# Kernel tuning notes

Hardware: AMD Instinct MI355X
Metric: run time of the kernel (lower is better)

## Reference

```python
import jax, jax.numpy as jnp
import numpy as np

B, N, D, H = 32, 64, 64, 4
E = 4 * D
HD = E // H
EPS = 1e-10
TAU = 1.0


def _ln(x, g, b, eps=1e-5):
    m = x.mean(-1, keepdims=True)
    v = ((x - m) ** 2).mean(-1, keepdims=True)
    return (x - m) * jax.lax.rsqrt(v + eps) * g + b


def setup_inputs() -> dict:
    key = jax.random.key(0)
    ks = jax.random.split(key, 8)
    x = jax.random.normal(ks[0], (B, N, D), jnp.float32)
    A = jax.random.normal(ks[1], (B, N, N, 2 * D), jnp.float32)
    attn_mask = jax.random.randint(ks[2], (B, N, N), 0, 2).astype(jnp.int32)
    gumbel_u = jax.random.uniform(ks[3], (B, N, H, N), jnp.float32, minval=1e-6, maxval=1.0)
    in_proj_w = (jax.random.normal(ks[4], (3 * E, E), jnp.float32) * (E ** -0.5))
    in_proj_b = jnp.zeros((3 * E,), jnp.float32)
    w1 = jax.random.normal(ks[5], (HD, HD), jnp.float32) * (HD ** -0.5)
    b1 = jnp.zeros((HD,), jnp.float32)
    w2 = jax.random.normal(ks[6], (1, HD), jnp.float32) * (HD ** -0.5)
    b2 = jnp.zeros((1,), jnp.float32)
    return dict(x=x, A=A, attn_mask=attn_mask, gumbel_u=gumbel_u,
                ln_node_g=jnp.ones((D,), jnp.float32), ln_node_b=jnp.zeros((D,), jnp.float32),
                ln_edge_g=jnp.ones((2 * D,), jnp.float32), ln_edge_b=jnp.zeros((2 * D,), jnp.float32),
                in_proj_w=in_proj_w, in_proj_b=in_proj_b, w1=w1, b1=b1, w2=w2, b2=b2)


def reference(x, A, attn_mask, gumbel_u, ln_node_g, ln_node_b, ln_edge_g, ln_edge_b,
              in_proj_w, in_proj_b, w1, b1, w2, b2):
    b, n, d = x.shape
    e = 4 * d
    hd = e // H
    mask = attn_mask.astype(x.dtype)                      # (b, target, neighbor), 1/0
    ped = (mask.sum(-1) > 0).astype(x.dtype)[..., None]   # (b, n, 1)
    xn = _ln(x, ln_node_g, ln_node_b) * ped
    An = _ln(A, ln_edge_g, ln_edge_b) * jnp.transpose(mask, (0, 2, 1))[..., None]
    # broadcast concat: (b, neighbor, target, 4d)
    xneigh = jnp.broadcast_to(xn[:, :, None, :], (b, n, n, d))
    xtarg = jnp.broadcast_to(xn[:, None, :, :], (b, n, n, d))
    A4 = jnp.concatenate([xneigh, xtarg, An], axis=-1)
    Ap = jnp.transpose(A4, (0, 2, 1, 3))                  # (b, target, neighbor, 4d)
    # in-projection (torch MHA layout: rows [q; k; v])
    qkv = jnp.einsum('btme,fe->btmf', Ap, in_proj_w) + in_proj_b
    q, k, v = jnp.split(qkv, 3, axis=-1)
    q = q.reshape(b, n, n, H, hd) * (hd ** -0.5)
    k = k.reshape(b, n, n, H, hd)
    v = v.reshape(b, n, n, H, hd)
    scores = jnp.einsum('btjhd,btkhd->bthjk', q, k)       # per-target neighborhood attention
    m3 = mask[:, :, :, None] * mask[:, :, None, :]        # (b, t, j, k)
    w = jax.nn.softmax(scores, axis=-1) * m3[:, :, None, :, :]
    w = w / (w.sum(-1, keepdims=True) + EPS)
    A2 = jnp.einsum('bthjk,btkhd->bthjd', w, v)           # (b, target, head, neighbor, hd)
    hmid = jax.nn.relu(jnp.einsum('bthjd,od->bthjo', A2, w1) + b1)
    logits = (jnp.einsum('bthjo,xo->bthjx', hmid, w2) + b2)[..., 0]  # (b, t, h, j)
    em = jax.nn.softmax(logits, axis=-1) * mask[:, :, None, :]
    em = em / (em.sum(-1, keepdims=True) + EPS)
    g = -jnp.log(-jnp.log(gumbel_u + EPS) + EPS)
    sampled = jax.nn.softmax((jnp.log(em + EPS) + g) / TAU, axis=-1)
    return em, sampled
```

## Files before the change

### kernel.cpp

```cpp
#include <hip/hip_runtime.h>
#include <hip/hip_bf16.h>
#include <math.h>


typedef __attribute__((ext_vector_type(8))) short short8;
typedef __attribute__((ext_vector_type(4))) short short4v;
typedef __attribute__((ext_vector_type(4))) float f32x4;

__device__ __forceinline__ short f2b(float f) {
  return (short)__builtin_bit_cast(unsigned short, __float2bfloat16(f));
}

#define WCS 136
#define TS  72

#define OFF_WC 0
#define OFF_A2 9216
#define OFF_RB 18432
#define OFF_RC 27648
#define OFF_F  36864
#define LDS_BYTES 39424

__global__ __launch_bounds__(256) void k_node_ln(
    const float* __restrict__ x, const int* __restrict__ mask,
    const float* __restrict__ g, const float* __restrict__ bb,
    float* __restrict__ xn) {
  int tid = threadIdx.x;
  int row = blockIdx.x * 4 + (tid >> 6);
  int lane = tid & 63;
  float v = x[row * 64 + lane];
  float s = v;
#pragma unroll
  for (int m = 1; m < 64; m <<= 1) s += __shfl_xor(s, m, 64);
  float mean = s * (1.0f / 64.0f);
  float dv = v - mean;
  float s2 = dv * dv;
#pragma unroll
  for (int m = 1; m < 64; m <<= 1) s2 += __shfl_xor(s2, m, 64);
  float rstd = rsqrtf(s2 * (1.0f / 64.0f) + 1e-5f);
  float msum = (float)mask[row * 64 + lane];
#pragma unroll
  for (int m = 1; m < 64; m <<= 1) msum += __shfl_xor(msum, m, 64);
  float ped = (msum > 0.0f) ? 1.0f : 0.0f;
  xn[row * 64 + lane] = (dv * rstd * g[lane] + bb[lane]) * ped;
}

__global__ __launch_bounds__(256) void k_t12(
    const float* __restrict__ xn, const float* __restrict__ W,
    const float* __restrict__ bias, float* __restrict__ T1s, float* __restrict__ T2) {
  __shared__ __align__(16) float sx[8 * 64];
  int tid = threadIdx.x;
  int r0 = blockIdx.x * 8;
#pragma unroll
  for (int u = 0; u < 2; ++u) {
    int idx = tid + 256 * u;
    sx[idx] = xn[r0 * 64 + idx];
  }
  __syncthreads();
#pragma unroll
  for (int ff = 0; ff < 3; ++ff) {
    int f = tid + 256 * ff;
    float acc1[8], acc2[8];
#pragma unroll
    for (int r = 0; r < 8; ++r) { acc1[r] = 0.f; acc2[r] = 0.f; }
    for (int e4 = 0; e4 < 64; e4 += 4) {
      float4 wa = *(const float4*)&W[f * 256 + e4];
      float4 wb = *(const float4*)&W[f * 256 + 64 + e4];
#pragma unroll
      for (int r = 0; r < 8; ++r) {
        float4 xv = *(const float4*)&sx[r * 64 + e4];
        acc1[r] += wa.x * xv.x + wa.y * xv.y + wa.z * xv.z + wa.w * xv.w;
        acc2[r] += wb.x * xv.x + wb.y * xv.y + wb.z * xv.z + wb.w * xv.w;
      }
    }
    float bv = bias[f];
    int p = f >> 8, hh = (f >> 6) & 3, dcol = f & 63;
#pragma unroll
    for (int r = 0; r < 8; ++r) {
      int m = r0 + r;
      int bb2 = m >> 6, mm = m & 63;
      int wv_ = mm >> 4;
      int lane, reg;
      if (p < 2) {
        lane = ((dcol >> 2) & 3) * 16 + (mm & 15);
        reg = (dcol >> 4) * 4 + (dcol & 3);
      } else {
        lane = ((mm >> 2) & 3) * 16 + (dcol & 15);
        reg = (dcol >> 4) * 4 + (mm & 3);
      }
      T1s[(size_t)((((bb2 * 3 + p) * 4 + hh) * 4 + wv_) * 64 + lane) * 16 + reg] =
          acc1[r];
      T2[m * 768 + f] = acc2[r] + bv;
    }
  }
}

__global__ __launch_bounds__(256) void k_wb(const float* __restrict__ W,
                                            const float* __restrict__ w1,
                                            short* __restrict__ Wb,
                                            short* __restrict__ w1b) {
  int idx = blockIdx.x * 256 + threadIdx.x;
  if (idx < 12288) {
    int f = idx >> 4, gi = idx & 15;
    const float* src = &W[(size_t)f * 256 + 128 + gi * 8];
    short8 o;
#pragma unroll
    for (int i = 0; i < 8; ++i) o[i] = f2b(src[i]);
    *(short8*)&Wb[f * 128 + gi * 8] = o;
  } else if (idx < 12288 + 512) {
    int g2 = idx - 12288;
    int f = g2 >> 3, gi = g2 & 7;
    const float* src = &w1[f * 64 + gi * 8];
    short8 o;
#pragma unroll
    for (int i = 0; i < 8; ++i) o[i] = f2b(src[i]);
    *(short8*)&w1b[f * 64 + gi * 8] = o;
  }
}

__global__ __launch_bounds__(256, 4) void k_main(
    const float* __restrict__ A, const int* __restrict__ mask,
    const float* __restrict__ gu, const float* __restrict__ leg,
    const float* __restrict__ leb, const float* __restrict__ b1g,
    const float* __restrict__ w2g, const float* __restrict__ b2g,
    const float* __restrict__ T1s, const float* __restrict__ T2,
    const short* __restrict__ Wb, const short* __restrict__ w1b,
    float* __restrict__ out) {
  __shared__ __align__(16) unsigned char smem[LDS_BYTES];
  short* sWc = (short*)(smem + OFF_WC);
  short* sQ  = (short*)(smem + OFF_WC);
  short* sWt = (short*)(smem + OFF_WC);
  short* sA2 = (short*)(smem + OFF_A2);
  short* sK  = (short*)(smem + OFF_RB);
  short* sVT = (short*)(smem + OFF_RC);
  float* sF  = (float*)(smem + OFF_F);

  int tid = threadIdx.x;
  int bid0 = blockIdx.x;
  int wg = (bid0 & 7) * 256 + (bid0 >> 3);
  int t = wg & 63, b = wg >> 6;
  int bt = b * 64 + t;
  int wave = tid >> 6, lane = tid & 63, lr = lane & 15, lh = lane >> 4;

  if (tid < 64) sF[192 + tid] = (float)mask[bt * 64 + tid];
  else if (tid < 128) sF[256 + tid - 64] = b1g[tid - 64];
  else if (tid < 192) sF[320 + tid - 128] = w2g[tid - 128];

  short8 af[4];
  {
    int m0 = wave * 16 + lr;
    const float* Ar = A + ((size_t)((b * 64 + m0) * 64 + t)) * 128;
    float4 a4[8];
#pragma unroll
    for (int ks = 0; ks < 4; ++ks) {
      a4[2 * ks]     = *(const float4*)&Ar[ks * 32 + lh * 8];
      a4[2 * ks + 1] = *(const float4*)&Ar[ks * 32 + lh * 8 + 4];
    }
    float s = 0.f, s2 = 0.f;
#pragma unroll
    for (int q = 0; q < 8; ++q) {
      float4 u0 = a4[q];
      s += u0.x + u0.y + u0.z + u0.w;
      s2 += u0.x * u0.x + u0.y * u0.y + u0.z * u0.z + u0.w * u0.w;
    }
    s += __shfl_xor(s, 16, 64);  s += __shfl_xor(s, 32, 64);
    s2 += __shfl_xor(s2, 16, 64); s2 += __shfl_xor(s2, 32, 64);
    float mean = s * (1.0f / 128.0f);
    float var = s2 * (1.0f / 128.0f) - mean * mean;
    float rstd = rsqrtf(var + 1e-5f);
    float mv = (float)mask[bt * 64 + m0];
#pragma unroll
    for (int ks = 0; ks < 4; ++ks) {
      float4 g0 = *(const float4*)&leg[ks * 32 + lh * 8];
      float4 g1 = *(const float4*)&leg[ks * 32 + lh * 8 + 4];
      float4 c0 = *(const float4*)&leb[ks * 32 + lh * 8];
      float4 c1 = *(const float4*)&leb[ks * 32 + lh * 8 + 4];
      float gg[8] = {g0.x, g0.y, g0.z, g0.w, g1.x, g1.y, g1.z, g1.w};
      float cc[8] = {c0.x, c0.y, c0.z, c0.w, c1.x, c1.y, c1.z, c1.w};
      float4 u0 = a4[2 * ks], u1 = a4[2 * ks + 1];
      float vv[8] = {u0.x, u0.y, u0.z, u0.w, u1.x, u1.y, u1.z, u1.w};
#pragma unroll
      for (int i = 0; i < 8; ++i)
        af[ks][i] = f2b(((vv[i] - mean) * rstd * gg[i] + cc[i]) * mv);
    }
  }

#pragma unroll 1
  for (int h = 0; h < 4; ++h) {
    __syncthreads();
    if (tid < 192) sF[tid] = T2[bt * 768 + (tid >> 6) * 256 + h * 64 + (tid & 63)];

#pragma unroll
    for (int pp = 0; pp < 3; ++pp) {
      const int p = (pp + 1) % 3;
      const int Fbase = p * 256 + h * 64;
#pragma unroll
      for (int u = 0; u < 4; ++u) {
        int idx = tid + 256 * u;
        int dR = idx >> 4, gi = idx & 15;
        *(short8*)&sWc[dR * WCS + gi * 8] =
            *(const short8*)&Wb[(size_t)(Fbase + dR) * 128 + gi * 8];
      }
      float4 t1f[4];
#pragma unroll
      for (int nt = 0; nt < 4; ++nt)
        t1f[nt] = *(const float4*)&T1s[
            (size_t)((((b * 3 + p) * 4 + h) * 4 + wave) * 64 + lane) * 16 + nt * 4];
      __syncthreads();
      f32x4 acc[4];
#pragma unroll
      for (int nt = 0; nt < 4; ++nt) {
        acc[nt][0] = t1f[nt].x; acc[nt][1] = t1f[nt].y;
        acc[nt][2] = t1f[nt].z; acc[nt][3] = t1f[nt].w;
      }
      if (p == 2) {
#pragma unroll
        for (int ks = 0; ks < 4; ++ks)
#pragma unroll
          for (int nt = 0; nt < 4; ++nt) {
            short8 bf = *(const short8*)&sWc[(nt * 16 + lr) * WCS + ks * 32 + lh * 8];
            acc[nt] = __builtin_amdgcn_mfma_f32_16x16x32_bf16(af[ks], bf, acc[nt], 0, 0, 0);
          }
      } else {
#pragma unroll
        for (int ks = 0; ks < 4; ++ks)
#pragma unroll
          for (int nt = 0; nt < 4; ++nt) {
            short8 bf = *(const short8*)&sWc[(nt * 16 + lr) * WCS + ks * 32 + lh * 8];
            acc[nt] = __builtin_amdgcn_mfma_f32_16x16x32_bf16(bf, af[ks], acc[nt], 0, 0, 0);
          }
      }
      if (p == 0) __syncthreads();
      if (p == 2) {
        float t2v[4];
#pragma unroll
        for (int nt = 0; nt < 4; ++nt) t2v[nt] = sF[128 + nt * 16 + lr];
#pragma unroll
        for (int nt = 0; nt < 4; ++nt) {
          short4v vp;
#pragma unroll
          for (int r = 0; r < 4; ++r) vp[r] = f2b(acc[nt][r] + t2v[nt]);
          *(short4v*)&sVT[(nt * 16 + lr) * TS + wave * 16 + lh * 4] = vp;
        }
      } else {
        float scale = (p == 0) ? 0.125f : 1.0f;
        short* dst = (p == 0) ? sQ : sK;
#pragma unroll
        for (int nt = 0; nt < 4; ++nt) {
          float4 t24 = *(const float4*)&sF[p * 64 + nt * 16 + lh * 4];
          float tv[4] = {t24.x, t24.y, t24.z, t24.w};
          short4v qp;
#pragma unroll
          for (int r = 0; r < 4; ++r) qp[r] = f2b((acc[nt][r] + tv[r]) * scale);
          *(short4v*)&dst[(wave * 16 + lr) * TS + nt * 16 + lh * 4] = qp;
        }
      }
      if (p != 0) __syncthreads();
    }

    {
      f32x4 sc[4] = {};
#pragma unroll
      for (int ks = 0; ks < 2; ++ks) {
        short8 qf = *(const short8*)&sQ[(wave * 16 + lr) * TS + ks * 32 + lh * 8];
#pragma unroll
        for (int nt = 0; nt < 4; ++nt) {
          short8 kf = *(const short8*)&sK[(nt * 16 + lr) * TS + ks * 32 + lh * 8];
          sc[nt] = __builtin_amdgcn_mfma_f32_16x16x32_bf16(kf, qf, sc[nt], 0, 0, 0);
        }
      }
      float mj = sF[192 + wave * 16 + lr];
      float mx = sc[0][0];
#pragma unroll
      for (int nt = 0; nt < 4; ++nt)
#pragma unroll
        for (int r = 0; r < 4; ++r) mx = fmaxf(mx, sc[nt][r]);
      mx = fmaxf(mx, __shfl_xor(mx, 16, 64));
      mx = fmaxf(mx, __shfl_xor(mx, 32, 64));
      float pv[4][4], mkv[4][4], Zf = 0.f, S = 0.f;
#pragma unroll
      for (int nt = 0; nt < 4; ++nt) {
        float4 mk4 = *(const float4*)&sF[192 + nt * 16 + lh * 4];
        float mk[4] = {mk4.x, mk4.y, mk4.z, mk4.w};
#pragma unroll
        for (int r = 0; r < 4; ++r) {
          float e = __expf(sc[nt][r] - mx);
          pv[nt][r] = e;
          mkv[nt][r] = mk[r];
          Zf += e;
          S += e * mk[r];
        }
      }
      Zf += __shfl_xor(Zf, 16, 64); Zf += __shfl_xor(Zf, 32, 64);
      S  += __shfl_xor(S, 16, 64);  S  += __shfl_xor(S, 32, 64);
      float inv = mj / (S + 1e-10f * Zf);
#pragma unroll
      for (int nt = 0; nt < 4; ++nt) {
        short4v wp;
#pragma unroll
        for (int r = 0; r < 4; ++r) wp[r] = f2b(pv[nt][r] * mkv[nt][r] * inv);
        *(short4v*)&sWt[(wave * 16 + lr) * TS + nt * 16 + lh * 4] = wp;
      }
    }

    {
      f32x4 a2[4] = {};
#pragma unroll
      for (int ks = 0; ks < 2; ++ks) {
        short8 wf = *(const short8*)&sWt[(wave * 16 + lr) * TS + ks * 32 + lh * 8];
#pragma unroll
        for (int nt = 0; nt < 4; ++nt) {
          short8 vf = *(const short8*)&sVT[(nt * 16 + lr) * TS + ks * 32 + lh * 8];
          a2[nt] = __builtin_amdgcn_mfma_f32_16x16x32_bf16(vf, wf, a2[nt], 0, 0, 0);
        }
      }
#pragma unroll
      for (int nt = 0; nt < 4; ++nt) {
        short4v ap;
#pragma unroll
        for (int r = 0; r < 4; ++r) ap[r] = f2b(a2[nt][r]);
        *(short4v*)&sA2[(wave * 16 + lr) * TS + nt * 16 + lh * 4] = ap;
      }
    }

    {
      f32x4 hm[4] = {};
#pragma unroll
      for (int ks = 0; ks < 2; ++ks) {
        short8 a2f = *(const short8*)&sA2[(wave * 16 + lr) * TS + ks * 32 + lh * 8];
#pragma unroll
        for (int nt = 0; nt < 4; ++nt) {
          short8 wf = *(const short8*)&w1b[(nt * 16 + lr) * 64 + ks * 32 + lh * 8];
          hm[nt] = __builtin_amdgcn_mfma_f32_16x16x32_bf16(wf, a2f, hm[nt], 0, 0, 0);
        }
      }
      float pp_ = 0.f;
#pragma unroll
      for (int nt = 0; nt < 4; ++nt) {
        float4 b14 = *(const float4*)&sF[256 + nt * 16 + lh * 4];
        float4 w24 = *(const float4*)&sF[320 + nt * 16 + lh * 4];
        float bb4[4] = {b14.x, b14.y, b14.z, b14.w};
        float ww4[4] = {w24.x, w24.y, w24.z, w24.w};
#pragma unroll
        for (int r = 0; r < 4; ++r)
          pp_ += fmaxf(hm[nt][r] + bb4[r], 0.f) * ww4[r];
      }
      pp_ += __shfl_xor(pp_, 16, 64);
      pp_ += __shfl_xor(pp_, 32, 64);
      if (lh == 0) sF[384 + h * 64 + wave * 16 + lr] = pp_;
    }
  }
  __syncthreads();

  {
    int hh = wave, j = lane;
    float l = sF[384 + hh * 64 + j] + b2g[0];
    float mjv = sF[192 + j];
    float mx = l;
#pragma unroll
    for (int mm = 1; mm < 64; mm <<= 1) mx = fmaxf(mx, __shfl_xor(mx, mm, 64));
    float pv = __expf(l - mx);
    float Z = pv;
#pragma unroll
    for (int mm = 1; mm < 64; mm <<= 1) Z += __shfl_xor(Z, mm, 64);
    float ep = (pv / Z) * mjv;
    float S = ep;
#pragma unroll
    for (int mm = 1; mm < 64; mm <<= 1) S += __shfl_xor(S, mm, 64);
    float em = ep / (S + 1e-10f);
    float u = gu[((size_t)bt * 4 + hh) * 64 + j];
    float gg = -__logf(-__logf(u + 1e-10f) + 1e-10f);
    float l2 = __logf(em + 1e-10f) + gg;
    float mx2 = l2;
#pragma unroll
    for (int mm = 1; mm < 64; mm <<= 1) mx2 = fmaxf(mx2, __shfl_xor(mx2, mm, 64));
    float p2 = __expf(l2 - mx2);
    float Z2 = p2;
#pragma unroll
    for (int mm = 1; mm < 64; mm <<= 1) Z2 += __shfl_xor(Z2, mm, 64);
    float smp = p2 / Z2;
    size_t o = ((size_t)bt * 4 + hh) * 64 + j;
    out[o] = em;
    out[524288 + o] = smp;
  }
}

extern "C" void kernel_launch(void* const* d_in, const int* in_sizes, int n_in,
                              void* d_out, int out_size, void* d_ws, size_t ws_size,
                              hipStream_t stream) {
  const float* x    = (const float*)d_in[0];
  const float* A    = (const float*)d_in[1];
  const int*   mask = (const int*)d_in[2];
  const float* gu   = (const float*)d_in[3];
  const float* lng  = (const float*)d_in[4];
  const float* lnb  = (const float*)d_in[5];
  const float* leg  = (const float*)d_in[6];
  const float* leb  = (const float*)d_in[7];
  const float* W    = (const float*)d_in[8];
  const float* bias = (const float*)d_in[9];
  const float* w1   = (const float*)d_in[10];
  const float* b1   = (const float*)d_in[11];
  const float* w2   = (const float*)d_in[12];
  const float* b2   = (const float*)d_in[13];
  float* out = (float*)d_out;
  float* ws  = (float*)d_ws;

  float* xn  = ws;
  float* T1s = xn + 131072;
  float* T2  = T1s + 1572864;
  short* Wb  = (short*)(T2 + 1572864);
  short* w1b = Wb + 98304;

  k_wb<<<50, 256, 0, stream>>>(W, w1, Wb, w1b);
  k_node_ln<<<512, 256, 0, stream>>>(x, mask, lng, lnb, xn);
  k_t12<<<256, 256, 0, stream>>>(xn, W, bias, T1s, T2);
  k_main<<<2048, 256, 0, stream>>>(A, mask, gu, leg, leb, b1, w2, b2,
                                   T1s, T2, Wb, w1b, out);
}
```

Measured before the change: 128.6 us.

## Process two targets per workgroup to reuse staged weight tiles

Each workgroup of k_main now handles two adjacent target nodes instead of one, so every weight chunk staged in LDS feeds twice as many MFMAs. The grid is halved, LDS use grows to about 59 KB, and launch bounds drop to 2 blocks per CU. The goal is to amortize the per-head global-to-LDS weight loads and barriers, at the cost of higher register and LDS pressure and lower occupancy.

```diff
diff --git a/kernel.cpp b/kernel.cpp
--- a/kernel.cpp
+++ b/kernel.cpp
@@ -14,12 +14,10 @@
 #define WCS 136
 #define TS  72
 
-#define OFF_WC 0
-#define OFF_A2 9216
-#define OFF_RB 18432
-#define OFF_RC 27648
-#define OFF_F  36864
-#define LDS_BYTES 39424
+#define OFF_K0  18432
+#define OFF_VT0 36864
+#define OFF_F   55296
+#define LDS_BYTES 59904
 
 __global__ __launch_bounds__(256) void k_node_ln(
     const float* __restrict__ x, const int* __restrict__ mask,
@@ -118,7 +116,7 @@
   }
 }
 
-__global__ __launch_bounds__(256, 4) void k_main(
+__global__ __launch_bounds__(256, 2) void k_main(
     const float* __restrict__ A, const int* __restrict__ mask,
     const float* __restrict__ gu, const float* __restrict__ leg,
     const float* __restrict__ leb, const float* __restrict__ b1g,
@@ -127,48 +125,49 @@
     const short* __restrict__ Wb, const short* __restrict__ w1b,
     float* __restrict__ out) {
   __shared__ __align__(16) unsigned char smem[LDS_BYTES];
-  short* sWc = (short*)(smem + OFF_WC);
-  short* sQ  = (short*)(smem + OFF_WC);
-  short* sWt = (short*)(smem + OFF_WC);
-  short* sA2 = (short*)(smem + OFF_A2);
-  short* sK  = (short*)(smem + OFF_RB);
-  short* sVT = (short*)(smem + OFF_RC);
+  short* sWc = (short*)smem;
   float* sF  = (float*)(smem + OFF_F);
 
   int tid = threadIdx.x;
   int bid0 = blockIdx.x;
-  int wg = (bid0 & 7) * 256 + (bid0 >> 3);
-  int t = wg & 63, b = wg >> 6;
-  int bt = b * 64 + t;
+  int wg = (bid0 & 7) * 128 + (bid0 >> 3);
+  int tq = wg & 31, b = wg >> 5;
+  int t0 = tq * 2;
+  int bt0 = b * 64 + t0;
   int wave = tid >> 6, lane = tid & 63, lr = lane & 15, lh = lane >> 4;
 
-  if (tid < 64) sF[192 + tid] = (float)mask[bt * 64 + tid];
-  else if (tid < 128) sF[256 + tid - 64] = b1g[tid - 64];
-  else if (tid < 192) sF[320 + tid - 128] = w2g[tid - 128];
-
-  short8 af[4];
+  if (tid < 64) sF[384 + tid] = (float)mask[bt0 * 64 + tid];
+  else if (tid < 128) sF[448 + tid - 64] = (float)mask[(bt0 + 1) * 64 + tid - 64];
+  else if (tid < 192) sF[512 + tid - 128] = b1g[tid - 128];
+  else sF[576 + tid - 192] = w2g[tid - 192];
+
+  short8 af[2][4];
   {
     int m0 = wave * 16 + lr;
-    const float* Ar = A + ((size_t)((b * 64 + m0) * 64 + t)) * 128;
-    float4 a4[8];
-#pragma unroll
-    for (int ks = 0; ks < 4; ++ks) {
-      a4[2 * ks]     = *(const float4*)&Ar[ks * 32 + lh * 8];
-      a4[2 * ks + 1] = *(const float4*)&Ar[ks * 32 + lh * 8 + 4];
-    }
-    float s = 0.f, s2 = 0.f;
-#pragma unroll
-    for (int q = 0; q < 8; ++q) {
-      float4 u0 = a4[q];
-      s += u0.x + u0.y + u0.z + u0.w;
-      s2 += u0.x * u0.x + u0.y * u0.y + u0.z * u0.z + u0.w * u0.w;
-    }
-    s += __shfl_xor(s, 16, 64);  s += __shfl_xor(s, 32, 64);
-    s2 += __shfl_xor(s2, 16, 64); s2 += __shfl_xor(s2, 32, 64);
-    float mean = s * (1.0f / 128.0f);
-    float var = s2 * (1.0f / 128.0f) - mean * mean;
-    float rstd = rsqrtf(var + 1e-5f);
-    float mv = (float)mask[bt * 64 + m0];
+    float4 a4[2][8];
+    float mean[2], rstd[2], mv[2];
+#pragma unroll
+    for (int e = 0; e < 2; ++e) {
+      const float* Ar = A + ((size_t)((b * 64 + m0) * 64 + t0 + e)) * 128;
+#pragma unroll
+      for (int ks = 0; ks < 4; ++ks) {
+        a4[e][2 * ks]     = *(const float4*)&Ar[ks * 32 + lh * 8];
+        a4[e][2 * ks + 1] = *(const float4*)&Ar[ks * 32 + lh * 8 + 4];
+      }
+      float s = 0.f, s2 = 0.f;
+#pragma unroll
+      for (int q = 0; q < 8; ++q) {
+        float4 u0 = a4[e][q];
+        s += u0.x + u0.y + u0.z + u0.w;
+        s2 += u0.x * u0.x + u0.y * u0.y + u0.z * u0.z + u0.w * u0.w;
+      }
+      s += __shfl_xor(s, 16, 64);  s += __shfl_xor(s, 32, 64);
+      s2 += __shfl_xor(s2, 16, 64); s2 += __shfl_xor(s2, 32, 64);
+      mean[e] = s * (1.0f / 128.0f);
+      float var = s2 * (1.0f / 128.0f) - mean[e] * mean[e];
+      rstd[e] = rsqrtf(var + 1e-5f);
+      mv[e] = (float)mask[(bt0 + e) * 64 + m0];
+    }
 #pragma unroll
     for (int ks = 0; ks < 4; ++ks) {
       float4 g0 = *(const float4*)&leg[ks * 32 + lh * 8];
@@ -177,18 +176,25 @@
       float4 c1 = *(const float4*)&leb[ks * 32 + lh * 8 + 4];
       float gg[8] = {g0.x, g0.y, g0.z, g0.w, g1.x, g1.y, g1.z, g1.w};
       float cc[8] = {c0.x, c0.y, c0.z, c0.w, c1.x, c1.y, c1.z, c1.w};
-      float4 u0 = a4[2 * ks], u1 = a4[2 * ks + 1];
-      float vv[8] = {u0.x, u0.y, u0.z, u0.w, u1.x, u1.y, u1.z, u1.w};
-#pragma unroll
-      for (int i = 0; i < 8; ++i)
-        af[ks][i] = f2b(((vv[i] - mean) * rstd * gg[i] + cc[i]) * mv);
+#pragma unroll
+      for (int e = 0; e < 2; ++e) {
+        float4 u0 = a4[e][2 * ks], u1 = a4[e][2 * ks + 1];
+        float vv[8] = {u0.x, u0.y, u0.z, u0.w, u1.x, u1.y, u1.z, u1.w};
+#pragma unroll
+        for (int i = 0; i < 8; ++i)
+          af[e][ks][i] = f2b(((vv[i] - mean[e]) * rstd[e] * gg[i] + cc[i]) * mv[e]);
+      }
     }
   }
 
 #pragma unroll 1
   for (int h = 0; h < 4; ++h) {
     __syncthreads();
-    if (tid < 192) sF[tid] = T2[bt * 768 + (tid >> 6) * 256 + h * 64 + (tid & 63)];
+    if (tid < 192) sF[tid] = T2[bt0 * 768 + (tid >> 6) * 256 + h * 64 + (tid & 63)];
+    if (tid >= 64) {
+      int i2 = tid - 64;
+      sF[192 + i2] = T2[(bt0 + 1) * 768 + (i2 >> 6) * 256 + h * 64 + (i2 & 63)];
+    }
 
 #pragma unroll
     for (int pp = 0; pp < 3; ++pp) {
@@ -207,11 +213,12 @@
         t1f[nt] = *(const float4*)&T1s[
             (size_t)((((b * 3 + p) * 4 + h) * 4 + wave) * 64 + lane) * 16 + nt * 4];
       __syncthreads();
-      f32x4 acc[4];
+      f32x4 acc0[4], acc1[4];
 #pragma unroll
       for (int nt = 0; nt < 4; ++nt) {
-        acc[nt][0] = t1f[nt].x; acc[nt][1] = t1f[nt].y;
-        acc[nt][2] = t1f[nt].z; acc[nt][3] = t1f[nt].w;
+        acc0[nt][0] = t1f[nt].x; acc0[nt][1] = t1f[nt].y;
+        acc0[nt][2] = t1f[nt].z; acc0[nt][3] = t1f[nt].w;
+        acc1[nt] = acc0[nt];
       }
       if (p == 2) {
 #pragma unroll
@@ -219,7 +226,8 @@
 #pragma unroll
           for (int nt = 0; nt < 4; ++nt) {
             short8 bf = *(const short8*)&sWc[(nt * 16 + lr) * WCS + ks * 32 + lh * 8];
-            acc[nt] = __builtin_amdgcn_mfma_f32_16x16x32_bf16(af[ks], bf, acc[nt], 0, 0, 0);
+            acc0[nt] = __builtin_amdgcn_mfma_f32_16x16x32_bf16(af[0][ks], bf, acc0[nt], 0, 0, 0);
+            acc1[nt] = __builtin_amdgcn_mfma_f32_16x16x32_bf16(af[1][ks], bf, acc1[nt], 0, 0, 0);
           }
       } else {
 #pragma unroll
@@ -227,49 +235,57 @@
 #pragma unroll
           for (int nt = 0; nt < 4; ++nt) {
             short8 bf = *(const short8*)&sWc[(nt * 16 + lr) * WCS + ks * 32 + lh * 8];
-            acc[nt] = __builtin_amdgcn_mfma_f32_16x16x32_bf16(bf, af[ks], acc[nt], 0, 0, 0);
+            acc0[nt] = __builtin_amdgcn_mfma_f32_16x16x32_bf16(bf, af[0][ks], acc0[nt], 0, 0, 0);
+            acc1[nt] = __builtin_amdgcn_mfma_f32_16x16x32_bf16(bf, af[1][ks], acc1[nt], 0, 0, 0);
           }
       }
       if (p == 0) __syncthreads();
-      if (p == 2) {
-        float t2v[4];
-#pragma unroll
-        for (int nt = 0; nt < 4; ++nt) t2v[nt] = sF[128 + nt * 16 + lr];
+#pragma unroll
+      for (int e = 0; e < 2; ++e) {
+        const f32x4* acc = (e == 0) ? acc0 : acc1;
+        if (p == 2) {
+          short* sVTt = (short*)(smem + OFF_VT0 + e * 9216);
+#pragma unroll
+          for (int nt = 0; nt < 4; ++nt) {
+            float t2v = sF[e * 192 + 128 + nt * 16 + lr];
+            short4v vp;
+#pragma unroll
+            for (int r = 0; r < 4; ++r) vp[r] = f2b(acc[nt][r] + t2v);
+            *(short4v*)&sVTt[(nt * 16 + lr) * TS + wave * 16 + lh * 4] = vp;
+          }
+        } else {
+          float scale = (p == 0) ? 0.125f : 1.0f;
+          short* dst = (p == 0) ? (short*)(smem + e * 9216)
+                                : (short*)(smem + OFF_K0 + e * 9216);
+#pragma unroll
+          for (int nt = 0; nt < 4; ++nt) {
+            float4 t24 = *(const float4*)&sF[e * 192 + p * 64 + nt * 16 + lh * 4];
+            float tv[4] = {t24.x, t24.y, t24.z, t24.w};
+            short4v qp;
+#pragma unroll
+            for (int r = 0; r < 4; ++r) qp[r] = f2b((acc[nt][r] + tv[r]) * scale);
+            *(short4v*)&dst[(wave * 16 + lr) * TS + nt * 16 + lh * 4] = qp;
+          }
+        }
+      }
+      if (p != 0) __syncthreads();
+    }
+
+#pragma unroll
+    for (int e = 0; e < 2; ++e) {
+      short* sQt = (short*)(smem + e * 9216);
+      short* sKt = (short*)(smem + OFF_K0 + e * 9216);
+      f32x4 sc[4] = {};
+#pragma unroll
+      for (int ks = 0; ks < 2; ++ks) {
+        short8 qf = *(const short8*)&sQt[(wave * 16 + lr) * TS + ks * 32 + lh * 8];
 #pragma unroll
         for (int nt = 0; nt < 4; ++nt) {
-          short4v vp;
-#pragma unroll
-          for (int r = 0; r < 4; ++r) vp[r] = f2b(acc[nt][r] + t2v[nt]);
-          *(short4v*)&sVT[(nt * 16 + lr) * TS + wave * 16 + lh * 4] = vp;
-        }
-      } else {
-        float scale = (p == 0) ? 0.125f : 1.0f;
-        short* dst = (p == 0) ? sQ : sK;
-#pragma unroll
-        for (int nt = 0; nt < 4; ++nt) {
-          float4 t24 = *(const float4*)&sF[p * 64 + nt * 16 + lh * 4];
-          float tv[4] = {t24.x, t24.y, t24.z, t24.w};
-          short4v qp;
-#pragma unroll
-          for (int r = 0; r < 4; ++r) qp[r] = f2b((acc[nt][r] + tv[r]) * scale);
-          *(short4v*)&dst[(wave * 16 + lr) * TS + nt * 16 + lh * 4] = qp;
-        }
-      }
-      if (p != 0) __syncthreads();
-    }
-
-    {
-      f32x4 sc[4] = {};
-#pragma unroll
-      for (int ks = 0; ks < 2; ++ks) {
-        short8 qf = *(const short8*)&sQ[(wave * 16 + lr) * TS + ks * 32 + lh * 8];
-#pragma unroll
-        for (int nt = 0; nt < 4; ++nt) {
-          short8 kf = *(const short8*)&sK[(nt * 16 + lr) * TS + ks * 32 + lh * 8];
+          short8 kf = *(const short8*)&sKt[(nt * 16 + lr) * TS + ks * 32 + lh * 8];
           sc[nt] = __builtin_amdgcn_mfma_f32_16x16x32_bf16(kf, qf, sc[nt], 0, 0, 0);
         }
       }
-      float mj = sF[192 + wave * 16 + lr];
+      float mj = sF[384 + e * 64 + wave * 16 + lr];
       float mx = sc[0][0];
 #pragma unroll
       for (int nt = 0; nt < 4; ++nt)
@@ -280,15 +296,15 @@
       float pv[4][4], mkv[4][4], Zf = 0.f, S = 0.f;
 #pragma unroll
       for (int nt = 0; nt < 4; ++nt) {
-        float4 mk4 = *(const float4*)&sF[192 + nt * 16 + lh * 4];
+        float4 mk4 = *(const float4*)&sF[384 + e * 64 + nt * 16 + lh * 4];
         float mk[4] = {mk4.x, mk4.y, mk4.z, mk4.w};
 #pragma unroll
         for (int r = 0; r < 4; ++r) {
-          float e = __expf(sc[nt][r] - mx);
-          pv[nt][r] = e;
+          float ev = __expf(sc[nt][r] - mx);
+          pv[nt][r] = ev;
           mkv[nt][r] = mk[r];
-          Zf += e;
-          S += e * mk[r];
+          Zf += ev;
+          S += ev * mk[r];
         }
       }
       Zf += __shfl_xor(Zf, 16, 64); Zf += __shfl_xor(Zf, 32, 64);
@@ -299,18 +315,23 @@
         short4v wp;
 #pragma unroll
         for (int r = 0; r < 4; ++r) wp[r] = f2b(pv[nt][r] * mkv[nt][r] * inv);
-        *(short4v*)&sWt[(wave * 16 + lr) * TS + nt * 16 + lh * 4] = wp;
-      }
-    }
-
-    {
+        *(short4v*)&sQt[(wave * 16 + lr) * TS + nt * 16 + lh * 4] = wp;
+      }
+    }
+    __syncthreads();
+
+#pragma unroll
+    for (int e = 0; e < 2; ++e) {
+      short* sWtt = (short*)(smem + e * 9216);
+      short* sVTt = (short*)(smem + OFF_VT0 + e * 9216);
+      short* sA2t = (short*)(smem + OFF_K0 + e * 9216);
       f32x4 a2[4] = {};
 #pragma unroll
       for (int ks = 0; ks < 2; ++ks) {
-        short8 wf = *(const short8*)&sWt[(wave * 16 + lr) * TS + ks * 32 + lh * 8];
+        short8 wf = *(const short8*)&sWtt[(wave * 16 + lr) * TS + ks * 32 + lh * 8];
 #pragma unroll
         for (int nt = 0; nt < 4; ++nt) {
-          short8 vf = *(const short8*)&sVT[(nt * 16 + lr) * TS + ks * 32 + lh * 8];
+          short8 vf = *(const short8*)&sVTt[(nt * 16 + lr) * TS + ks * 32 + lh * 8];
           a2[nt] = __builtin_amdgcn_mfma_f32_16x16x32_bf16(vf, wf, a2[nt], 0, 0, 0);
         }
       }
@@ -319,15 +340,12 @@
         short4v ap;
 #pragma unroll
         for (int r = 0; r < 4; ++r) ap[r] = f2b(a2[nt][r]);
-        *(short4v*)&sA2[(wave * 16 + lr) * TS + nt * 16 + lh * 4] = ap;
-      }
-    }
-
-    {
+        *(short4v*)&sA2t[(wave * 16 + lr) * TS + nt * 16 + lh * 4] = ap;
+      }
       f32x4 hm[4] = {};
 #pragma unroll
       for (int ks = 0; ks < 2; ++ks) {
-        short8 a2f = *(const short8*)&sA2[(wave * 16 + lr) * TS + ks * 32 + lh * 8];
+        short8 a2f = *(const short8*)&sA2t[(wave * 16 + lr) * TS + ks * 32 + lh * 8];
 #pragma unroll
         for (int nt = 0; nt < 4; ++nt) {
           short8 wf = *(const short8*)&w1b[(nt * 16 + lr) * 64 + ks * 32 + lh * 8];
@@ -337,8 +355,8 @@
       float pp_ = 0.f;
 #pragma unroll
       for (int nt = 0; nt < 4; ++nt) {
-        float4 b14 = *(const float4*)&sF[256 + nt * 16 + lh * 4];
-        float4 w24 = *(const float4*)&sF[320 + nt * 16 + lh * 4];
+        float4 b14 = *(const float4*)&sF[512 + nt * 16 + lh * 4];
+        float4 w24 = *(const float4*)&sF[576 + nt * 16 + lh * 4];
         float bb4[4] = {b14.x, b14.y, b14.z, b14.w};
         float ww4[4] = {w24.x, w24.y, w24.z, w24.w};
 #pragma unroll
@@ -347,15 +365,17 @@
       }
       pp_ += __shfl_xor(pp_, 16, 64);
       pp_ += __shfl_xor(pp_, 32, 64);
-      if (lh == 0) sF[384 + h * 64 + wave * 16 + lr] = pp_;
+      if (lh == 0) sF[640 + (e * 4 + h) * 64 + wave * 16 + lr] = pp_;
     }
   }
   __syncthreads();
 
-  {
-    int hh = wave, j = lane;
-    float l = sF[384 + hh * 64 + j] + b2g[0];
-    float mjv = sF[192 + j];
+#pragma unroll
+  for (int it = 0; it < 2; ++it) {
+    int tile = it, hh = wave, j = lane;
+    int btx = bt0 + tile;
+    float l = sF[640 + (tile * 4 + hh) * 64 + j] + b2g[0];
+    float mjv = sF[384 + tile * 64 + j];
     float mx = l;
 #pragma unroll
     for (int mm = 1; mm < 64; mm <<= 1) mx = fmaxf(mx, __shfl_xor(mx, mm, 64));
@@ -368,7 +388,7 @@
 #pragma unroll
     for (int mm = 1; mm < 64; mm <<= 1) S += __shfl_xor(S, mm, 64);
     float em = ep / (S + 1e-10f);
-    float u = gu[((size_t)bt * 4 + hh) * 64 + j];
+    float u = gu[((size_t)btx * 4 + hh) * 64 + j];
     float gg = -__logf(-__logf(u + 1e-10f) + 1e-10f);
     float l2 = __logf(em + 1e-10f) + gg;
     float mx2 = l2;
@@ -379,7 +399,7 @@
 #pragma unroll
     for (int mm = 1; mm < 64; mm <<= 1) Z2 += __shfl_xor(Z2, mm, 64);
     float smp = p2 / Z2;
-    size_t o = ((size_t)bt * 4 + hh) * 64 + j;
+    size_t o = ((size_t)btx * 4 + hh) * 64 + j;
     out[o] = em;
     out[524288 + o] = smp;
   }
@@ -414,6 +434,6 @@
   k_wb<<<50, 256, 0, stream>>>(W, w1, Wb, w1b);
   k_node_ln<<<512, 256, 0, stream>>>(x, mask, lng, lnb, xn);
   k_t12<<<256, 256, 0, stream>>>(xn, W, bias, T1s, T2);
-  k_main<<<2048, 256, 0, stream>>>(A, mask, gu, leg, leb, b1, w2, b2,
+  k_main<<<1024, 256, 0, stream>>>(A, mask, gu, leg, leb, b1, w2, b2,
                                    T1s, T2, Wb, w1b, out);
 }
```

Result: faster. 119.0 us (-7.5%).

## Double-buffer weight tiles via async global-to-LDS loads with XOR swizzle

Applied to the files above, without the earlier changes.

Replaces the per-projection synchronous staging of the bf16 weight slice with double-buffered global_load_lds transfers. The next slice, the next T1 accumulator tile and the next head's T2 bias are prefetched while the current MFMA block runs. Padded weight rows are replaced by an XOR swizzle applied when the weights are converted, and several LDS buffers are reused to cut barriers per head. LDS use grows to about 63KB and the occupancy hint is dropped from the launch bounds, which may lower the number of resident workgroups.

```diff
diff --git a/kernel.cpp b/kernel.cpp
--- a/kernel.cpp
+++ b/kernel.cpp
@@ -11,15 +11,14 @@
   return (short)__builtin_bit_cast(unsigned short, __float2bfloat16(f));
 }
 
-#define WCS 136
-#define TS  72
-
-#define OFF_WC 0
-#define OFF_A2 9216
-#define OFF_RB 18432
-#define OFF_RC 27648
-#define OFF_F  36864
-#define LDS_BYTES 39424
+#define TS 72
+
+#define OFF_WCB 16384
+#define OFF_QW  32768
+#define OFF_RK  41984
+#define OFF_RV  51200
+#define OFF_F   60416
+#define LDS_BYTES 62976
 
 __global__ __launch_bounds__(256) void k_node_ln(
     const float* __restrict__ x, const int* __restrict__ mask,
@@ -83,10 +82,10 @@
       int lane, reg;
       if (p < 2) {
         lane = ((dcol >> 2) & 3) * 16 + (mm & 15);
-        reg = (dcol >> 4) * 4 + (dcol & 3);
+        reg  = (dcol >> 4) * 4 + (dcol & 3);
       } else {
         lane = ((mm >> 2) & 3) * 16 + (dcol & 15);
-        reg = (dcol >> 4) * 4 + (mm & 3);
+        reg  = (dcol >> 4) * 4 + (mm & 3);
       }
       T1s[(size_t)((((bb2 * 3 + p) * 4 + hh) * 4 + wv_) * 64 + lane) * 16 + reg] =
           acc1[r];
@@ -102,7 +101,8 @@
   int idx = blockIdx.x * 256 + threadIdx.x;
   if (idx < 12288) {
     int f = idx >> 4, gi = idx & 15;
-    const float* src = &W[(size_t)f * 256 + 128 + gi * 8];
+    int gs = gi ^ (f & 7);
+    const float* src = &W[(size_t)f * 256 + 128 + gs * 8];
     short8 o;
 #pragma unroll
     for (int i = 0; i < 8; ++i) o[i] = f2b(src[i]);
@@ -118,7 +118,24 @@
   }
 }
 
-__global__ __launch_bounds__(256, 4) void k_main(
+__device__ __forceinline__ void stage_wc(const short* __restrict__ Wb, int Fbase,
+                                         unsigned char* bufb, int wave, int lane) {
+  const short* src = Wb + (size_t)Fbase * 128 + wave * 2048 + lane * 8;
+  unsigned char* dst = bufb + wave * 4096 + lane * 16;
+#pragma unroll
+  for (int q = 0; q < 4; ++q) {
+    __builtin_amdgcn_global_load_lds(
+        (const __attribute__((address_space(1))) unsigned int*)(src + q * 512),
+        (__attribute__((address_space(3))) unsigned int*)(dst + q * 1024),
+        16, 0, 0);
+  }
+}
+
+__device__ __forceinline__ short8 wcread(const short* buf, int row, int g) {
+  return *(const short8*)&buf[row * 128 + ((g ^ (row & 7)) << 3)];
+}
+
+__global__ __launch_bounds__(256) void k_main(
     const float* __restrict__ A, const int* __restrict__ mask,
     const float* __restrict__ gu, const float* __restrict__ leg,
     const float* __restrict__ leb, const float* __restrict__ b1g,
@@ -127,12 +144,9 @@
     const short* __restrict__ Wb, const short* __restrict__ w1b,
     float* __restrict__ out) {
   __shared__ __align__(16) unsigned char smem[LDS_BYTES];
-  short* sWc = (short*)(smem + OFF_WC);
-  short* sQ  = (short*)(smem + OFF_WC);
-  short* sWt = (short*)(smem + OFF_WC);
-  short* sA2 = (short*)(smem + OFF_A2);
-  short* sK  = (short*)(smem + OFF_RB);
-  short* sVT = (short*)(smem + OFF_RC);
+  short* sQ  = (short*)(smem + OFF_QW);
+  short* sK  = (short*)(smem + OFF_RK);
+  short* sVT = (short*)(smem + OFF_RV);
   float* sF  = (float*)(smem + OFF_F);
 
   int tid = threadIdx.x;
@@ -145,6 +159,14 @@
   if (tid < 64) sF[192 + tid] = (float)mask[bt * 64 + tid];
   else if (tid < 128) sF[256 + tid - 64] = b1g[tid - 64];
   else if (tid < 192) sF[320 + tid - 128] = w2g[tid - 128];
+  if (tid < 192) sF[tid] = T2[bt * 768 + (tid >> 6) * 256 + (tid & 63)];
+
+  stage_wc(Wb, 256, smem, wave, lane);
+  float4 t1n[4];
+#pragma unroll
+  for (int nt = 0; nt < 4; ++nt)
+    t1n[nt] = *(const float4*)&T1s[
+        (size_t)((((b * 3 + 1) * 4 + 0) * 4 + wave) * 64 + lane) * 16 + nt * 4];
 
   short8 af[4];
   {
@@ -185,88 +207,87 @@
     }
   }
 
+  float t2n = 0.f;
+
 #pragma unroll 1
   for (int h = 0; h < 4; ++h) {
-    __syncthreads();
-    if (tid < 192) sF[tid] = T2[bt * 768 + (tid >> 6) * 256 + h * 64 + (tid & 63)];
-
 #pragma unroll
     for (int pp = 0; pp < 3; ++pp) {
-      const int p = (pp + 1) % 3;
-      const int Fbase = p * 256 + h * 64;
-#pragma unroll
-      for (int u = 0; u < 4; ++u) {
-        int idx = tid + 256 * u;
-        int dR = idx >> 4, gi = idx & 15;
-        *(short8*)&sWc[dR * WCS + gi * 8] =
-            *(const short8*)&Wb[(size_t)(Fbase + dR) * 128 + gi * 8];
-      }
-      float4 t1f[4];
-#pragma unroll
-      for (int nt = 0; nt < 4; ++nt)
-        t1f[nt] = *(const float4*)&T1s[
-            (size_t)((((b * 3 + p) * 4 + h) * 4 + wave) * 64 + lane) * 16 + nt * 4];
       __syncthreads();
+      int cur = (h + pp) & 1;
+      const short* bufc = (const short*)(smem + (cur ? OFF_WCB : 0));
+      unsigned char* bufn = smem + (cur ? 0 : OFF_WCB);
+      if (pp == 0)      stage_wc(Wb, 512 + h * 64, bufn, wave, lane);
+      else if (pp == 1) stage_wc(Wb, h * 64, bufn, wave, lane);
+      else if (h < 3)   stage_wc(Wb, 256 + (h + 1) * 64, bufn, wave, lane);
+      float4 t1c[4];
+#pragma unroll
+      for (int nt = 0; nt < 4; ++nt) t1c[nt] = t1n[nt];
+      if (!(pp == 2 && h == 3)) {
+        int pn = (pp == 0) ? 2 : (pp == 1) ? 0 : 1;
+        int hn = (pp == 2) ? h + 1 : h;
+#pragma unroll
+        for (int nt = 0; nt < 4; ++nt)
+          t1n[nt] = *(const float4*)&T1s[
+              (size_t)((((b * 3 + pn) * 4 + hn) * 4 + wave) * 64 + lane) * 16 + nt * 4];
+      }
       f32x4 acc[4];
 #pragma unroll
       for (int nt = 0; nt < 4; ++nt) {
-        acc[nt][0] = t1f[nt].x; acc[nt][1] = t1f[nt].y;
-        acc[nt][2] = t1f[nt].z; acc[nt][3] = t1f[nt].w;
-      }
-      if (p == 2) {
-#pragma unroll
-        for (int ks = 0; ks < 4; ++ks)
-#pragma unroll
-          for (int nt = 0; nt < 4; ++nt) {
-            short8 bf = *(const short8*)&sWc[(nt * 16 + lr) * WCS + ks * 32 + lh * 8];
+        acc[nt][0] = t1c[nt].x; acc[nt][1] = t1c[nt].y;
+        acc[nt][2] = t1c[nt].z; acc[nt][3] = t1c[nt].w;
+      }
+#pragma unroll
+      for (int ks = 0; ks < 4; ++ks)
+#pragma unroll
+        for (int nt = 0; nt < 4; ++nt) {
+          short8 bf = wcread(bufc, nt * 16 + lr, ks * 4 + lh);
+          if (pp == 1)
             acc[nt] = __builtin_amdgcn_mfma_f32_16x16x32_bf16(af[ks], bf, acc[nt], 0, 0, 0);
-          }
+          else
+            acc[nt] = __builtin_amdgcn_mfma_f32_16x16x32_bf16(bf, af[ks], acc[nt], 0, 0, 0);
+        }
+      if (pp == 0) {
+#pragma unroll
+        for (int nt = 0; nt < 4; ++nt) {
+          float4 t24 = *(const float4*)&sF[64 + nt * 16 + lh * 4];
+          float tv[4] = {t24.x, t24.y, t24.z, t24.w};
+          short4v kp;
+#pragma unroll
+          for (int r = 0; r < 4; ++r) kp[r] = f2b(acc[nt][r] + tv[r]);
+          *(short4v*)&sK[(wave * 16 + lr) * TS + nt * 16 + lh * 4] = kp;
+        }
+      } else if (pp == 1) {
+#pragma unroll
+        for (int nt = 0; nt < 4; ++nt) {
+          float t2v = sF[128 + nt * 16 + lr];
+          short4v vp;
+#pragma unroll
+          for (int r = 0; r < 4; ++r) vp[r] = f2b(acc[nt][r] + t2v);
+          *(short4v*)&sVT[(nt * 16 + lr) * TS + wave * 16 + lh * 4] = vp;
+        }
       } else {
 #pragma unroll
-        for (int ks = 0; ks < 4; ++ks)
-#pragma unroll
-          for (int nt = 0; nt < 4; ++nt) {
-            short8 bf = *(const short8*)&sWc[(nt * 16 + lr) * WCS + ks * 32 + lh * 8];
-            acc[nt] = __builtin_amdgcn_mfma_f32_16x16x32_bf16(bf, af[ks], acc[nt], 0, 0, 0);
-          }
-      }
-      if (p == 0) __syncthreads();
-      if (p == 2) {
-        float t2v[4];
-#pragma unroll
-        for (int nt = 0; nt < 4; ++nt) t2v[nt] = sF[128 + nt * 16 + lr];
-#pragma unroll
-        for (int nt = 0; nt < 4; ++nt) {
-          short4v vp;
-#pragma unroll
-          for (int r = 0; r < 4; ++r) vp[r] = f2b(acc[nt][r] + t2v[nt]);
-          *(short4v*)&sVT[(nt * 16 + lr) * TS + wave * 16 + lh * 4] = vp;
-        }
-      } else {
-        float scale = (p == 0) ? 0.125f : 1.0f;
-        short* dst = (p == 0) ? sQ : sK;
-#pragma unroll
-        for (int nt = 0; nt < 4; ++nt) {
-          float4 t24 = *(const float4*)&sF[p * 64 + nt * 16 + lh * 4];
+        for (int nt = 0; nt < 4; ++nt) {
+          float4 t24 = *(const float4*)&sF[nt * 16 + lh * 4];
           float tv[4] = {t24.x, t24.y, t24.z, t24.w};
           short4v qp;
 #pragma unroll
-          for (int r = 0; r < 4; ++r) qp[r] = f2b((acc[nt][r] + tv[r]) * scale);
-          *(short4v*)&dst[(wave * 16 + lr) * TS + nt * 16 + lh * 4] = qp;
-        }
-      }
-      if (p != 0) __syncthreads();
+          for (int r = 0; r < 4; ++r) qp[r] = f2b((acc[nt][r] + tv[r]) * 0.125f);
+          *(short4v*)&sQ[(wave * 16 + lr) * TS + nt * 16 + lh * 4] = qp;
+        }
+      }
     }
 
     {
       f32x4 sc[4] = {};
 #pragma unroll
       for (int ks = 0; ks < 2; ++ks) {
-        short8 qf = *(const short8*)&sQ[(wave * 16 + lr) * TS + ks * 32 + lh * 8];
+        short8 qfr = *(const short8*)&sQ[(wave * 16 + lr) * TS + ks * 32 + lh * 8];
 #pragma unroll
         for (int nt = 0; nt < 4; ++nt) {
           short8 kf = *(const short8*)&sK[(nt * 16 + lr) * TS + ks * 32 + lh * 8];
-          sc[nt] = __builtin_amdgcn_mfma_f32_16x16x32_bf16(kf, qf, sc[nt], 0, 0, 0);
+          sc[nt] = __builtin_amdgcn_mfma_f32_16x16x32_bf16(kf, qfr, sc[nt], 0, 0, 0);
         }
       }
       float mj = sF[192 + wave * 16 + lr];
@@ -284,11 +305,11 @@
         float mk[4] = {mk4.x, mk4.y, mk4.z, mk4.w};
 #pragma unroll
         for (int r = 0; r < 4; ++r) {
-          float e = __expf(sc[nt][r] - mx);
-          pv[nt][r] = e;
+          float ev = __expf(sc[nt][r] - mx);
+          pv[nt][r] = ev;
           mkv[nt][r] = mk[r];
-          Zf += e;
-          S += e * mk[r];
+          Zf += ev;
+          S += ev * mk[r];
         }
       }
       Zf += __shfl_xor(Zf, 16, 64); Zf += __shfl_xor(Zf, 32, 64);
@@ -299,19 +320,23 @@
         short4v wp;
 #pragma unroll
         for (int r = 0; r < 4; ++r) wp[r] = f2b(pv[nt][r] * mkv[nt][r] * inv);
-        *(short4v*)&sWt[(wave * 16 + lr) * TS + nt * 16 + lh * 4] = wp;
-      }
-    }
+        *(short4v*)&sQ[(wave * 16 + lr) * TS + nt * 16 + lh * 4] = wp;
+      }
+    }
+    if (h < 3 && tid < 192)
+      t2n = T2[bt * 768 + (tid >> 6) * 256 + (h + 1) * 64 + (tid & 63)];
+    __syncthreads();
+    if (h < 3 && tid < 192) sF[tid] = t2n;
 
     {
       f32x4 a2[4] = {};
 #pragma unroll
       for (int ks = 0; ks < 2; ++ks) {
-        short8 wf = *(const short8*)&sWt[(wave * 16 + lr) * TS + ks * 32 + lh * 8];
+        short8 wfr = *(const short8*)&sQ[(wave * 16 + lr) * TS + ks * 32 + lh * 8];
 #pragma unroll
         for (int nt = 0; nt < 4; ++nt) {
           short8 vf = *(const short8*)&sVT[(nt * 16 + lr) * TS + ks * 32 + lh * 8];
-          a2[nt] = __builtin_amdgcn_mfma_f32_16x16x32_bf16(vf, wf, a2[nt], 0, 0, 0);
+          a2[nt] = __builtin_amdgcn_mfma_f32_16x16x32_bf16(vf, wfr, a2[nt], 0, 0, 0);
         }
       }
 #pragma unroll
@@ -319,19 +344,16 @@
         short4v ap;
 #pragma unroll
         for (int r = 0; r < 4; ++r) ap[r] = f2b(a2[nt][r]);
-        *(short4v*)&sA2[(wave * 16 + lr) * TS + nt * 16 + lh * 4] = ap;
-      }
-    }
-
-    {
+        *(short4v*)&sK[(wave * 16 + lr) * TS + nt * 16 + lh * 4] = ap;
+      }
       f32x4 hm[4] = {};
 #pragma unroll
       for (int ks = 0; ks < 2; ++ks) {
-        short8 a2f = *(const short8*)&sA2[(wave * 16 + lr) * TS + ks * 32 + lh * 8];
-#pragma unroll
-        for (int nt = 0; nt < 4; ++nt) {
-          short8 wf = *(const short8*)&w1b[(nt * 16 + lr) * 64 + ks * 32 + lh * 8];
-          hm[nt] = __builtin_amdgcn_mfma_f32_16x16x32_bf16(wf, a2f, hm[nt], 0, 0, 0);
+        short8 a2f = *(const short8*)&sK[(wave * 16 + lr) * TS + ks * 32 + lh * 8];
+#pragma unroll
+        for (int nt = 0; nt < 4; ++nt) {
+          short8 wf1 = *(const short8*)&w1b[(nt * 16 + lr) * 64 + ks * 32 + lh * 8];
+          hm[nt] = __builtin_amdgcn_mfma_f32_16x16x32_bf16(wf1, a2f, hm[nt], 0, 0, 0);
         }
       }
       float pp_ = 0.f;
```

Result: slower. 140.1 us (+8.9%).
